# Optimization experiments

Measured on AMD Instinct MI355X. Metric: run time of the kernel, lower is better.

Reference implementation:

```python
import jax, jax.numpy as jnp
import numpy as np

DEPTH = 8  # dilation_depth; dilation for layer i is 2**(i % DEPTH)


def causal_conv(x, w, b, dilation):
    # x: [B,C,T], w: [O,I,K] -> causal dilated conv, output [B,O,T]
    pad = (w.shape[-1] - 1) * dilation
    xp = jnp.pad(x, ((0, 0), (0, 0), (pad, 0)))
    y = jax.lax.conv_general_dilated(
        xp, w, window_strides=(1,), padding='VALID',
        rhs_dilation=(dilation,), dimension_numbers=('NCW', 'OIW', 'NCW'))
    return y + b[None, :, None]


def conv1x1(x, w, b):
    # x: [B,C,T], w: [O,C] -> [B,O,T]
    return jnp.einsum('oc,bct->bot', w, x) + b[None, :, None]


def setup_inputs() -> dict:
    key = jax.random.key(0)
    ks = jax.random.split(key, 20)
    B, T, F, E = 16, 2048, 32, 16
    R, S, O, NOUT, L = 256, 128, 64, 24, 32  # residual, skip, out_size, n_output, layers
    s = 0.05
    return {
        'X_batch': jax.random.normal(ks[0], (B, T, F), jnp.float32),
        'X_batch_ex': jax.random.normal(ks[1], (B, E), jnp.float32),
        'w_in': jax.random.normal(ks[2], (R, F, 2), jnp.float32) * s,
        'b_in': jax.random.normal(ks[3], (R,), jnp.float32) * s,
        'w_filter': jax.random.normal(ks[4], (L, R, R, 2), jnp.float32) * s,
        'b_filter': jax.random.normal(ks[5], (L, R), jnp.float32) * s,
        'w_gate': jax.random.normal(ks[6], (L, R, R, 2), jnp.float32) * s,
        'b_gate': jax.random.normal(ks[7], (L, R), jnp.float32) * s,
        'w_res': jax.random.normal(ks[8], (L, R, R), jnp.float32) * s,
        'b_res': jax.random.normal(ks[9], (L, R), jnp.float32) * s,
        'w_skip': jax.random.normal(ks[10], (L, S, R), jnp.float32) * s,
        'b_skip': jax.random.normal(ks[11], (L, S), jnp.float32) * s,
        'w_out1': jax.random.normal(ks[12], (O, S), jnp.float32) * s,
        'b_out1': jax.random.normal(ks[13], (O,), jnp.float32) * s,
        'w_out2': jax.random.normal(ks[14], (O, O), jnp.float32) * s,
        'b_out2': jax.random.normal(ks[15], (O,), jnp.float32) * s,
        'w_lin': jax.random.normal(ks[16], (NOUT, O + E), jnp.float32) * s,
        'b_lin': jax.random.normal(ks[17], (NOUT,), jnp.float32) * s,
    }


def reference(X_batch, X_batch_ex, w_in, b_in, w_filter, b_filter, w_gate, b_gate,
              w_res, b_res, w_skip, b_skip, w_out1, b_out1, w_out2, b_out2,
              w_lin, b_lin):
    # [B,T,F] -> [B,F,T]
    x = jnp.transpose(X_batch, (0, 2, 1))
    x = causal_conv(x, w_in, b_in, 1)
    L = w_filter.shape[0]
    skip_sum = jnp.zeros((x.shape[0], w_skip.shape[1], x.shape[2]), x.dtype)
    for i in range(L):
        d = 2 ** (i % DEPTH)
        f = jnp.tanh(causal_conv(x, w_filter[i], b_filter[i], d))
        g = jax.nn.sigmoid(causal_conv(x, w_gate[i], b_gate[i], d))
        fx = conv1x1(f * g, w_res[i], b_res[i])
        skip_sum = skip_sum + conv1x1(fx, w_skip[i], b_skip[i])
        x = fx + x
    out = jax.nn.relu(skip_sum)
    out = jax.nn.relu(conv1x1(out, w_out1, b_out1))
    out = conv1x1(out, w_out2, b_out2)          # [B,O,T]
    h = out[:, :, -1]                            # last timestep, [B,O]
    h = jnp.concatenate([h, X_batch_ex], axis=1)
    h = jax.nn.relu(h)
    return h @ w_lin.T + b_lin                   # [B, n_output]
```

## Files before the change

kernel.cpp:

```cpp
#include <hip/hip_runtime.h>
#include <cmath>

#define TBUF 1024
#define RCH  256

typedef __bf16 bf16x8 __attribute__((ext_vector_type(8)));
typedef float  f32x4  __attribute__((ext_vector_type(4)));

__device__ inline unsigned short f2bf(float f) {
  unsigned u = __builtin_bit_cast(unsigned, f);
  u += 0x7FFFu + ((u >> 16) & 1u);
  return (unsigned short)(u >> 16);
}
__device__ inline float bf2f(unsigned short h) {
  unsigned u = ((unsigned)h) << 16;
  return __builtin_bit_cast(float, u);
}

__global__ __launch_bounds__(256) void prep(
    const float* __restrict__ wf, const float* __restrict__ wg,
    const float* __restrict__ wr, const float* __restrict__ wsk,
    const float* __restrict__ w_in,
    unsigned short* __restrict__ Wb, unsigned short* __restrict__ Wrb,
    float* __restrict__ wskT, float* __restrict__ w2)
{
  const int bid = blockIdx.x;
  const int tid = threadIdx.x;
  if (bid < 16384) {
    int idx = bid * 256 + tid;
    int c  = idx & 255;
    int op = (idx >> 8) & 511;
    int i  = idx >> 17;
    int o  = op & 255;
    const float* src = (op < 256) ? wf : wg;
    const float2 v = *(const float2*)&src[(((size_t)i * 256 + o) * 256 + c) << 1];
    unsigned short* dst = Wb + ((size_t)i * 512 + op) * 512;
    dst[c]       = f2bf(v.y);
    dst[256 + c] = f2bf(v.x);
  } else if (bid < 18432) {
    int idx = (bid - 16384) * 256 + tid;
    float4 v = ((const float4*)wr)[idx];
    uint2 o;
    o.x = (unsigned)f2bf(v.x) | ((unsigned)f2bf(v.y) << 16);
    o.y = (unsigned)f2bf(v.z) | ((unsigned)f2bf(v.w) << 16);
    ((uint2*)Wrb)[idx] = o;
  } else if (bid < 22528) {
    int idx = (bid - 18432) * 256 + tid;
    int s = idx & 127;
    int c = (idx >> 7) & 255;
    int i = idx >> 15;
    wskT[idx] = wsk[(i * 128 + s) * 256 + c];
  } else {
    int idx = (bid - 22528) * 256 + tid;
    int r = idx & 255;
    int fk = idx >> 8;
    int f = fk & 31, k = fk >> 5;
    w2[idx] = w_in[r * 64 + f * 2 + k];
  }
}

__global__ __launch_bounds__(256) void in_conv(
    const float* __restrict__ X, const float* __restrict__ w2,
    const float* __restrict__ b_in, unsigned short* __restrict__ xbb,
    unsigned short* __restrict__ xlo)
{
  const int bid   = blockIdx.x;
  const int b     = bid & 15;
  const int chunk = bid >> 4;
  const int r     = threadIdx.x;
  __shared__ float Xs[17][32];
  const int tt0 = chunk << 4;
  const int t0  = tt0 + 1024;
  for (int idx = r; idx < 17 * 32; idx += 256) {
    int row = idx >> 5, f = idx & 31;
    Xs[row][f] = X[((size_t)b * 2048 + (t0 - 1 + row)) * 32 + f];
  }
  __syncthreads();
  float w0[32], w1[32];
  #pragma unroll
  for (int f = 0; f < 32; ++f) {
    w0[f] = w2[f * 256 + r];
    w1[f] = w2[(32 + f) * 256 + r];
  }
  const float bias = b_in[r];
  float4 prev[8], cur[8];
  #pragma unroll
  for (int q = 0; q < 8; ++q) prev[q] = *(const float4*)&Xs[0][q * 4];
  #pragma unroll
  for (int j = 0; j < 16; ++j) {
    #pragma unroll
    for (int q = 0; q < 8; ++q) cur[q] = *(const float4*)&Xs[j + 1][q * 4];
    float a = bias;
    #pragma unroll
    for (int q = 0; q < 8; ++q) {
      a = fmaf(w0[q*4+0], prev[q].x, a); a = fmaf(w1[q*4+0], cur[q].x, a);
      a = fmaf(w0[q*4+1], prev[q].y, a); a = fmaf(w1[q*4+1], cur[q].y, a);
      a = fmaf(w0[q*4+2], prev[q].z, a); a = fmaf(w1[q*4+2], cur[q].z, a);
      a = fmaf(w0[q*4+3], prev[q].w, a); a = fmaf(w1[q*4+3], cur[q].w, a);
    }
    int tt = tt0 + j;
    size_t off = ((size_t)b * TBUF + tt) * RCH + r;
    if (tt < 3) { xbb[off] = 0; xlo[off] = 0; }
    else {
      unsigned short hn = f2bf(a);
      xbb[off] = hn;
      xlo[off] = f2bf(a - bf2f(hn));
    }
    #pragma unroll
    for (int q = 0; q < 8; ++q) prev[q] = cur[q];
  }
}

template<int NM>
__global__ __launch_bounds__(1024, 4) void layer_fused(
    const unsigned short* __restrict__ xbb_r, unsigned short* __restrict__ xbb_w,
    unsigned short* __restrict__ xlo,
    const unsigned short* __restrict__ Wb,
    const unsigned short* __restrict__ Wrb,
    const float* __restrict__ bF, const float* __restrict__ bG,
    const float* __restrict__ bR,
    int dd, int t_lo, float* __restrict__ fxs_i)
{
  __shared__ __align__(16) unsigned short As[NM * 16 * 520];
  const int bid  = blockIdx.x;
  const int b    = bid & 15;
  const int tile = bid >> 4;
  const int tid  = threadIdx.x;
  const int w    = tid >> 6;
  const int lane = tid & 63;
  const int l15  = lane & 15;
  const int lk8  = (lane >> 4) << 3;
  const int rr0  = (lane >> 4) << 2;
  const int tt0  = t_lo + tile * (NM * 16);
  const unsigned short* xB = xbb_r + ((size_t)b << 18);

  {
    const int c   = lane;
    const int tap = c >> 5;
    const int cg  = (c & 31) << 3;
    #pragma unroll
    for (int it = 0; it < NM; ++it) {
      int r = it * 16 + w;
      int tt = tt0 + r - tap * dd;
      tt = min(max(tt, 0), 1023);
      __builtin_amdgcn_global_load_lds(
          (const __attribute__((address_space(1))) unsigned int*)
              (xB + ((size_t)tt << 8) + cg),
          (__attribute__((address_space(3))) unsigned int*)
              ((char*)As + r * 1040),
          16, 0, 0);
    }
  }
  __syncthreads();

  f32x4 accf[NM] = {};
  f32x4 accg[NM] = {};
  const unsigned short* wf0 = Wb + (size_t)(16 * w + l15) * 512 + lk8;
  const unsigned short* wg0 = wf0 + (size_t)256 * 512;
  #pragma unroll 4
  for (int kc = 0; kc < 16; ++kc) {
    const int k0 = kc * 32;
    uint4 ubf0 = *(const uint4*)(wf0 + k0);
    uint4 ubg0 = *(const uint4*)(wg0 + k0);
    const int colb = (k0 + lk8) * 2;
    bf16x8 a[NM];
    #pragma unroll
    for (int mf = 0; mf < NM; ++mf)
      a[mf] = *(const bf16x8*)((const char*)As + (mf * 16 + l15) * 1040 + colb);
    bf16x8 vf0 = __builtin_bit_cast(bf16x8, ubf0);
    bf16x8 vg0 = __builtin_bit_cast(bf16x8, ubg0);
    #pragma unroll
    for (int mf = 0; mf < NM; ++mf) {
      accf[mf] = __builtin_amdgcn_mfma_f32_16x16x32_bf16(a[mf], vf0, accf[mf], 0, 0, 0);
      accg[mf] = __builtin_amdgcn_mfma_f32_16x16x32_bf16(a[mf], vg0, accg[mf], 0, 0, 0);
    }
  }

  const int col = 16 * w + l15;
  float hi_pre[NM][4];
  #pragma unroll
  for (int mf = 0; mf < NM; ++mf)
    #pragma unroll
    for (int j = 0; j < 4; ++j) {
      int row = mf * 16 + rr0 + j;
      hi_pre[mf][j] = bf2f(*(const unsigned short*)((const char*)As + row * 1040 + col * 2));
    }
  __syncthreads();

  unsigned short* Zs = As;
  const float bfv = bF[col];
  const float bgv = bG[col];
  #pragma unroll
  for (int mf = 0; mf < NM; ++mf)
    #pragma unroll
    for (int j = 0; j < 4; ++j) {
      int row = mf * 16 + rr0 + j;
      float pf = accf[mf][j] + bfv;
      float pg = accg[mf][j] + bgv;
      float e2 = __expf(2.f * pf);
      float th = 1.f - 2.f / (e2 + 1.f);
      float sg = 1.f / (1.f + __expf(-pg));
      *(unsigned short*)((char*)Zs + row * 528 + col * 2) = f2bf(th * sg);
    }
  __syncthreads();

  unsigned short* xL = xlo + ((size_t)b << 18);
  float lo_pre[NM][4];
  #pragma unroll
  for (int mf = 0; mf < NM; ++mf)
    #pragma unroll
    for (int j = 0; j < 4; ++j) {
      int tt = min(tt0 + mf * 16 + rr0 + j, 1023);
      lo_pre[mf][j] = bf2f(xL[((size_t)tt << 8) + col]);
    }

  f32x4 acc[NM] = {};
  const unsigned short* wr0 = Wrb + (size_t)(16 * w + l15) * 256 + lk8;
  #pragma unroll 4
  for (int kc = 0; kc < 8; ++kc) {
    uint4 ur0 = *(const uint4*)(wr0 + kc * 32);
    const int colb = (kc * 32 + lk8) * 2;
    bf16x8 a[NM];
    #pragma unroll
    for (int mf = 0; mf < NM; ++mf)
      a[mf] = *(const bf16x8*)((const char*)Zs + (mf * 16 + l15) * 528 + colb);
    bf16x8 v0 = __builtin_bit_cast(bf16x8, ur0);
    #pragma unroll
    for (int mf = 0; mf < NM; ++mf)
      acc[mf] = __builtin_amdgcn_mfma_f32_16x16x32_bf16(a[mf], v0, acc[mf], 0, 0, 0);
  }

  const float brv = bR[col];
  unsigned short* xBb = xbb_w + ((size_t)b << 18);
  #pragma unroll
  for (int mf = 0; mf < NM; ++mf)
    #pragma unroll
    for (int j = 0; j < 4; ++j) {
      int tt = tt0 + mf * 16 + rr0 + j;
      if (tt > 1023) continue;
      size_t off = ((size_t)tt << 8) + col;
      float fx = acc[mf][j] + brv;
      float xn = (hi_pre[mf][j] + lo_pre[mf][j]) + fx;
      unsigned short hn = f2bf(xn);
      xBb[off] = hn;
      xL[off]  = f2bf(xn - bf2f(hn));
      if (tt == 1023) fxs_i[(size_t)b * 256 + col] = fx;
    }
}

__global__ __launch_bounds__(128) void skip_partial(
    const float* __restrict__ fxs, const float* __restrict__ wskT,
    const float* __restrict__ b_skip, float* __restrict__ part)
{
  int i = blockIdx.x, b = blockIdx.y, s = threadIdx.x;
  __shared__ float fxsh[256];
  fxsh[s]       = fxs[((size_t)i * 16 + b) * 256 + s];
  fxsh[s + 128] = fxs[((size_t)i * 16 + b) * 256 + s + 128];
  __syncthreads();
  float a = b_skip[i * 128 + s];
  const float* wp = wskT + (size_t)i * 256 * 128 + s;
  #pragma unroll 4
  for (int c = 0; c < 256; c++)
    a = fmaf(wp[c * 128], fxsh[c], a);
  part[((size_t)i * 16 + b) * 128 + s] = a;
}

__global__ __launch_bounds__(128) void head2(
    const float* __restrict__ part, const float* __restrict__ w_o1,
    const float* __restrict__ b_o1, const float* __restrict__ w_o2,
    const float* __restrict__ b_o2, const float* __restrict__ w_lin,
    const float* __restrict__ b_lin, const float* __restrict__ Xex,
    float* __restrict__ out)
{
  int b = blockIdx.x, tid = threadIdx.x;
  __shared__ float sk[128];
  __shared__ float h1[64];
  __shared__ float hc[80];
  float a = 0.f;
  for (int i = 0; i < 32; i++) a += part[((size_t)i * 16 + b) * 128 + tid];
  sk[tid] = fmaxf(a, 0.f);
  __syncthreads();
  if (tid < 64) {
    float a1 = b_o1[tid];
    for (int s = 0; s < 128; s++) a1 = fmaf(w_o1[tid * 128 + s], sk[s], a1);
    h1[tid] = fmaxf(a1, 0.f);
  }
  __syncthreads();
  if (tid < 64) {
    float a2 = b_o2[tid];
    for (int j = 0; j < 64; j++) a2 = fmaf(w_o2[tid * 64 + j], h1[j], a2);
    hc[tid] = fmaxf(a2, 0.f);
  }
  if (tid >= 64 && tid < 80) hc[tid] = fmaxf(Xex[b * 16 + (tid - 64)], 0.f);
  __syncthreads();
  if (tid < 24) {
    float a3 = b_lin[tid];
    for (int j = 0; j < 80; j++) a3 = fmaf(w_lin[tid * 80 + j], hc[j], a3);
    out[b * 24 + tid] = a3;
  }
}

extern "C" void kernel_launch(void* const* d_in, const int* in_sizes, int n_in,
                              void* d_out, int out_size, void* d_ws, size_t ws_size,
                              hipStream_t stream)
{
  (void)in_sizes; (void)n_in; (void)out_size; (void)ws_size;
  const float* X     = (const float*)d_in[0];
  const float* Xex   = (const float*)d_in[1];
  const float* w_in  = (const float*)d_in[2];
  const float* b_in  = (const float*)d_in[3];
  const float* w_f   = (const float*)d_in[4];
  const float* b_f   = (const float*)d_in[5];
  const float* w_g   = (const float*)d_in[6];
  const float* b_g   = (const float*)d_in[7];
  const float* w_r   = (const float*)d_in[8];
  const float* b_r   = (const float*)d_in[9];
  const float* w_s   = (const float*)d_in[10];
  const float* b_s   = (const float*)d_in[11];
  const float* w_o1  = (const float*)d_in[12];
  const float* b_o1  = (const float*)d_in[13];
  const float* w_o2  = (const float*)d_in[14];
  const float* b_o2  = (const float*)d_in[15];
  const float* w_lin = (const float*)d_in[16];
  const float* b_lin = (const float*)d_in[17];

  float* ws   = (float*)d_ws;
  float* wskT = ws;
  float* fxs  = wskT + 1048576;
  float* part = fxs  + 131072;
  float* w2   = part + 65536;
  unsigned short* Wb   = (unsigned short*)(w2 + 16384);
  unsigned short* Wrb  = Wb   + 8388608;
  unsigned short* xbbA = Wrb  + 2097152;
  unsigned short* xbbB = xbbA + 4194304;
  unsigned short* xlo  = xbbB + 4194304;

  prep<<<22592, 256, 0, stream>>>(w_f, w_g, w_r, w_s, w_in, Wb, Wrb, wskT, w2);
  in_conv<<<1024, 256, 0, stream>>>(X, w2, b_in, xbbA, xlo);

  static const int wI[33] = {1021,1020,1018,1014,1006,990,958,894,
                             766,765,763,759,751,735,703,639,
                             511,510,508,504,496,480,448,384,
                             256,255,253,249,241,225,193,129,1};
  for (int i = 0; i < 32; i++) {
    int dd    = 1 << (i & 7);
    int Wout  = wI[i + 1];
    int t_lo  = TBUF - Wout;
    unsigned short* xin  = (i & 1) ? xbbB : xbbA;
    unsigned short* xout = (i & 1) ? xbbA : xbbB;
    const unsigned short* WbL  = Wb  + (size_t)i * 512 * 512;
    const unsigned short* WrbL = Wrb + (size_t)i * 256 * 256;
    const float* bFi = b_f + i * 256;
    const float* bGi = b_g + i * 256;
    const float* bRi = b_r + i * 256;
    float* fxi = fxs + (size_t)i * 16 * 256;
    if (Wout >= 520) {
      int tiles = (Wout + 63) / 64;
      layer_fused<4><<<tiles * 16, 1024, 0, stream>>>(
          xin, xout, xlo, WbL, WrbL, bFi, bGi, bRi, dd, t_lo, fxi);
    } else if (Wout >= 260) {
      int tiles = (Wout + 31) / 32;
      layer_fused<2><<<tiles * 16, 1024, 0, stream>>>(
          xin, xout, xlo, WbL, WrbL, bFi, bGi, bRi, dd, t_lo, fxi);
    } else {
      int tiles = (Wout + 15) / 16;
      layer_fused<1><<<tiles * 16, 1024, 0, stream>>>(
          xin, xout, xlo, WbL, WrbL, bFi, bGi, bRi, dd, t_lo, fxi);
    }
  }
  skip_partial<<<dim3(32, 16), 128, 0, stream>>>(fxs, wskT, b_s, part);
  head2<<<16, 128, 0, stream>>>(part, w_o1, b_o1, w_o2, b_o2, w_lin, b_lin, Xex, (float*)d_out);
}
```

Baseline: 904.8 us.

## Prefetch weight fragments one K-step ahead and pick tile rows per layer width

Weight loads in both MFMA loops are software-pipelined: the next K-chunk's global fragment is loaded while the current one feeds the MFMAs, and the first fragments are issued before the barrier. The residual low-part loads are hoisted ahead of the gate epilogue so their latency overlaps other work. The host now chooses the NM tile template (including a new NM=3) from ceil(Wout/256), so each layer gets about 16 tiles times 16 batches and less padding waste. This costs more live registers per thread, which could lower occupancy.

```diff
diff --git a/kernel.cpp b/kernel.cpp
--- a/kernel.cpp
+++ b/kernel.cpp
@@ -151,24 +151,31 @@
           16, 0, 0);
     }
   }
+
+  const unsigned short* wf0 = Wb + (size_t)(16 * w + l15) * 512 + lk8;
+  const unsigned short* wg0 = wf0 + (size_t)256 * 512;
+  const unsigned short* wr0 = Wrb + (size_t)(16 * w + l15) * 256 + lk8;
+  uint4 nbf = *(const uint4*)(wf0);
+  uint4 nbg = *(const uint4*)(wg0);
+  uint4 nr0 = *(const uint4*)(wr0);
   __syncthreads();
 
   f32x4 accf[NM] = {};
   f32x4 accg[NM] = {};
-  const unsigned short* wf0 = Wb + (size_t)(16 * w + l15) * 512 + lk8;
-  const unsigned short* wg0 = wf0 + (size_t)256 * 512;
   #pragma unroll 4
   for (int kc = 0; kc < 16; ++kc) {
-    const int k0 = kc * 32;
-    uint4 ubf0 = *(const uint4*)(wf0 + k0);
-    uint4 ubg0 = *(const uint4*)(wg0 + k0);
-    const int colb = (k0 + lk8) * 2;
+    uint4 cbf = nbf, cbg = nbg;
+    if (kc < 15) {
+      nbf = *(const uint4*)(wf0 + (kc + 1) * 32);
+      nbg = *(const uint4*)(wg0 + (kc + 1) * 32);
+    }
+    const int colb = (kc * 32 + lk8) * 2;
     bf16x8 a[NM];
     #pragma unroll
     for (int mf = 0; mf < NM; ++mf)
       a[mf] = *(const bf16x8*)((const char*)As + (mf * 16 + l15) * 1040 + colb);
-    bf16x8 vf0 = __builtin_bit_cast(bf16x8, ubf0);
-    bf16x8 vg0 = __builtin_bit_cast(bf16x8, ubg0);
+    bf16x8 vf0 = __builtin_bit_cast(bf16x8, cbf);
+    bf16x8 vg0 = __builtin_bit_cast(bf16x8, cbg);
     #pragma unroll
     for (int mf = 0; mf < NM; ++mf) {
       accf[mf] = __builtin_amdgcn_mfma_f32_16x16x32_bf16(a[mf], vf0, accf[mf], 0, 0, 0);
@@ -184,6 +191,16 @@
     for (int j = 0; j < 4; ++j) {
       int row = mf * 16 + rr0 + j;
       hi_pre[mf][j] = bf2f(*(const unsigned short*)((const char*)As + row * 1040 + col * 2));
+    }
+
+  unsigned short* xL = xlo + ((size_t)b << 18);
+  float lo_pre[NM][4];
+  #pragma unroll
+  for (int mf = 0; mf < NM; ++mf)
+    #pragma unroll
+    for (int j = 0; j < 4; ++j) {
+      int tt = min(tt0 + mf * 16 + rr0 + j, 1023);
+      lo_pre[mf][j] = bf2f(xL[((size_t)tt << 8) + col]);
     }
   __syncthreads();
 
@@ -204,27 +221,17 @@
     }
   __syncthreads();
 
-  unsigned short* xL = xlo + ((size_t)b << 18);
-  float lo_pre[NM][4];
-  #pragma unroll
-  for (int mf = 0; mf < NM; ++mf)
-    #pragma unroll
-    for (int j = 0; j < 4; ++j) {
-      int tt = min(tt0 + mf * 16 + rr0 + j, 1023);
-      lo_pre[mf][j] = bf2f(xL[((size_t)tt << 8) + col]);
-    }
-
   f32x4 acc[NM] = {};
-  const unsigned short* wr0 = Wrb + (size_t)(16 * w + l15) * 256 + lk8;
   #pragma unroll 4
   for (int kc = 0; kc < 8; ++kc) {
-    uint4 ur0 = *(const uint4*)(wr0 + kc * 32);
+    uint4 cr0 = nr0;
+    if (kc < 7) nr0 = *(const uint4*)(wr0 + (kc + 1) * 32);
     const int colb = (kc * 32 + lk8) * 2;
     bf16x8 a[NM];
     #pragma unroll
     for (int mf = 0; mf < NM; ++mf)
       a[mf] = *(const bf16x8*)((const char*)Zs + (mf * 16 + l15) * 528 + colb);
-    bf16x8 v0 = __builtin_bit_cast(bf16x8, ur0);
+    bf16x8 v0 = __builtin_bit_cast(bf16x8, cr0);
     #pragma unroll
     for (int mf = 0; mf < NM; ++mf)
       acc[mf] = __builtin_amdgcn_mfma_f32_16x16x32_bf16(a[mf], v0, acc[mf], 0, 0, 0);
@@ -354,18 +361,25 @@
     const float* bGi = b_g + i * 256;
     const float* bRi = b_r + i * 256;
     float* fxi = fxs + (size_t)i * 16 * 256;
-    if (Wout >= 520) {
-      int tiles = (Wout + 63) / 64;
-      layer_fused<4><<<tiles * 16, 1024, 0, stream>>>(
-          xin, xout, xlo, WbL, WrbL, bFi, bGi, bRi, dd, t_lo, fxi);
-    } else if (Wout >= 260) {
-      int tiles = (Wout + 31) / 32;
-      layer_fused<2><<<tiles * 16, 1024, 0, stream>>>(
-          xin, xout, xlo, WbL, WrbL, bFi, bGi, bRi, dd, t_lo, fxi);
-    } else {
-      int tiles = (Wout + 15) / 16;
-      layer_fused<1><<<tiles * 16, 1024, 0, stream>>>(
-          xin, xout, xlo, WbL, WrbL, bFi, bGi, bRi, dd, t_lo, fxi);
+    int NM = (Wout + 255) >> 8;
+    int tiles = (Wout + NM * 16 - 1) / (NM * 16);
+    switch (NM) {
+      case 4:
+        layer_fused<4><<<tiles * 16, 1024, 0, stream>>>(
+            xin, xout, xlo, WbL, WrbL, bFi, bGi, bRi, dd, t_lo, fxi);
+        break;
+      case 3:
+        layer_fused<3><<<tiles * 16, 1024, 0, stream>>>(
+            xin, xout, xlo, WbL, WrbL, bFi, bGi, bRi, dd, t_lo, fxi);
+        break;
+      case 2:
+        layer_fused<2><<<tiles * 16, 1024, 0, stream>>>(
+            xin, xout, xlo, WbL, WrbL, bFi, bGi, bRi, dd, t_lo, fxi);
+        break;
+      default:
+        layer_fused<1><<<tiles * 16, 1024, 0, stream>>>(
+            xin, xout, xlo, WbL, WrbL, bFi, bGi, bRi, dd, t_lo, fxi);
+        break;
     }
   }
   skip_partial<<<dim3(32, 16), 128, 0, stream>>>(fxs, wskT, b_s, part);
```

New measurement: 883.0 us. 1.02x faster.
